# Optimization experiments

Hardware: AMD Instinct MI355X
Metric: run time of the kernel (lower is better)

Reference implementation:

```python
import jax, jax.numpy as jnp
import numpy as np
import math

NC = 80
TOPK = 10
EPS = 1e-9
DIS = 2.5
BIG = 1e5


def _ciou(b1, b2, eps=EPS):
    # b1: (bs,1,A,4), b2: (bs,G,1,4) -> (bs,G,A)
    b1x1, b1y1, b1x2, b1y2 = b1[..., 0], b1[..., 1], b1[..., 2], b1[..., 3]
    b2x1, b2y1, b2x2, b2y2 = b2[..., 0], b2[..., 1], b2[..., 2], b2[..., 3]
    w1, h1 = b1x2 - b1x1, b1y2 - b1y1 + eps
    w2, h2 = b2x2 - b2x1, b2y2 - b2y1 + eps
    iw = jnp.clip(jnp.minimum(b1x2, b2x2) - jnp.maximum(b1x1, b2x1), 0.0)
    ih = jnp.clip(jnp.minimum(b1y2, b2y2) - jnp.maximum(b1y1, b2y1), 0.0)
    inter = iw * ih
    union = w1 * h1 + w2 * h2 - inter + eps
    iou = inter / union
    cw = jnp.maximum(b1x2, b2x2) - jnp.minimum(b1x1, b2x1)
    ch = jnp.maximum(b1y2, b2y2) - jnp.minimum(b1y1, b2y1)
    c2 = cw * cw + ch * ch + eps
    d2 = ((b2x1 + b2x2 - b1x1 - b1x2) ** 2 + (b2y1 + b2y2 - b1y1 - b1y2) ** 2) / 4.0
    v = (4.0 / math.pi ** 2) * (jnp.arctan(w2 / h2) - jnp.arctan(w1 / h1)) ** 2
    alpha = jax.lax.stop_gradient(v / (v - iou + (1.0 + eps)))
    return iou - (d2 / c2 + v * alpha)


def _cost_matrix(pred_boxes, gt_boxes, mask_gt, pred_scores, gt_labels):
    # geometric candidate masks
    pc = (pred_boxes[..., :2] + pred_boxes[..., 2:]) / 2.0  # (bs,A,2) anchor centers
    pce = pc[:, None, :, :]                                  # (bs,1,A,2)
    in_boxes = jnp.all(pce > gt_boxes[:, :, None, :2], -1) & jnp.all(gt_boxes[:, :, None, 2:] > pce, -1)
    gcen = (gt_boxes[..., :2] + gt_boxes[..., 2:]) / 2.0
    in_centers = jnp.all(pce > (gcen - DIS)[:, :, None, :], -1) & jnp.all((gcen + DIS)[:, :, None, :] > pce, -1)
    both = in_boxes & in_centers                             # (bs,G,A)

    ciou_val = _ciou(pred_boxes[:, None, :, :], gt_boxes[:, :, None, :])  # (bs,G,A)

    # summed BCE over classes against one-hot(gt_label), without (bs,G,A,nc) intermediate:
    # sum_c bce = -sum_c log(1-p_c) - (log p_y - log(1-p_y))
    p = jnp.clip(pred_scores, 1e-7, 1.0 - 1e-7)
    logp = jnp.log(p)
    log1mp = jnp.log1p(-p)
    S = -log1mp.sum(-1)                                      # (bs,A)
    delta = -(logp - log1mp)                                 # (bs,A,nc)
    per_lab = jnp.take_along_axis(jnp.transpose(delta, (0, 2, 1)), gt_labels[:, :, None], axis=1)  # (bs,G,A)
    cls_cost = S[:, None, :] + per_lab

    cost = cls_cost + 3.0 * ciou_val + BIG * (~both).astype(cost_dtype(pred_boxes))
    return cost


def cost_dtype(x):
    return x.dtype


def reference(pred_boxes, gt_boxes, mask_gt, pred_scores, gt_labels):
    cost = _cost_matrix(pred_boxes, gt_boxes, mask_gt, pred_scores, gt_labels)  # (bs,G,A)
    bs, G, A = cost.shape
    # per-GT bottom-k (lowest cost) candidate anchors
    _, idx = jax.lax.top_k(-cost, TOPK)                      # (bs,G,TOPK)
    b_ix = jnp.arange(bs)[:, None, None]
    g_ix = jnp.arange(G)[None, :, None]
    pt_mask = jnp.zeros((bs, G, A), dtype=bool).at[b_ix, g_ix, idx].set(True)
    pt_mask = pt_mask & mask_gt[:, :, None]
    # conflict resolution: anchors claimed by >1 GT go to the min-cost GT
    overlap = pt_mask.sum(1) > 1                             # (bs,A)
    pick = jnp.argmin(jnp.where(pt_mask, cost, jnp.inf), axis=1)  # (bs,A)
    pick_oh = jnp.arange(G)[None, :, None] == pick[:, None, :]    # (bs,G,A)
    final = jnp.where(overlap[:, None, :], pick_oh, pt_mask) & mask_gt[:, :, None]
    return final, cost


def setup_inputs() -> dict:
    key = jax.random.key(0)
    k = jax.random.split(key, 7)
    bs, A, G = 32, 8400, 64
    pc = jax.random.uniform(k[0], (bs, A, 2)) * 640.0
    pwh = jax.random.uniform(k[1], (bs, A, 2)) * 96.0 + 8.0
    pred_boxes = jnp.concatenate([pc - pwh / 2, pc + pwh / 2], -1)
    gc = jax.random.uniform(k[2], (bs, G, 2)) * 640.0
    gwh = jax.random.uniform(k[3], (bs, G, 2)) * 128.0 + 16.0
    gt_boxes = jnp.concatenate([gc - gwh / 2, gc + gwh / 2], -1)
    mask_gt = jax.random.uniform(k[4], (bs, G)) < 0.8
    pred_scores = jax.random.uniform(k[5], (bs, A, NC), minval=1e-4, maxval=1.0 - 1e-4)
    gt_labels = jax.random.randint(k[6], (bs, G), 0, NC, dtype=jnp.int32)
    return {"pred_boxes": pred_boxes, "gt_boxes": gt_boxes, "mask_gt": mask_gt,
            "pred_scores": pred_scores, "gt_labels": gt_labels}
```

## Files before the change

kernel.cpp:

```cpp
#include <hip/hip_runtime.h>
#include <math.h>

#define BS   32
#define A_N  8400
#define G_N  64
#define NC_N 80
#define TK   10
#define DROWS 44

static __device__ __forceinline__ bool lexless(float v1, int i1, float v2, int i2) {
    return (v1 < v2) || (v1 == v2 && i1 < i2);
}
static __device__ __forceinline__ float fdiv(float n, float d) {
    return n * __builtin_amdgcn_rcpf(d);
}

__global__ __launch_bounds__(256)
void k_cost(const float* __restrict__ pred_boxes,
            const float* __restrict__ gt_boxes,
            const float* __restrict__ pred_scores,
            const int*   __restrict__ gt_labels,
            float* __restrict__ cost)
{
    __shared__ float s_gx1[G_N], s_gy1[G_N], s_gx2[G_N], s_gy2[G_N];
    __shared__ float s_gsx[G_N], s_gsy[G_N];
    __shared__ float s_glx[G_N], s_gly[G_N], s_ghx[G_N], s_ghy[G_N];
    __shared__ float s_area2[G_N], s_atg[G_N];
    __shared__ int   s_lab[G_N];
    __shared__ int   s_ord[G_N];
    __shared__ int   s_pres[NC_N];
    __shared__ int   s_rank[NC_N];
    __shared__ float s_delta[DROWS * 256];

    const float EPSF = 1e-9f;
    const int t = threadIdx.x;
    const int b = blockIdx.y;
    const int a = blockIdx.x * 256 + t;

    if (t < G_N) {
        const float4 gb = ((const float4*)gt_boxes)[b * G_N + t];
        const float gx1 = gb.x, gy1 = gb.y, gx2 = gb.z, gy2 = gb.w;
        s_gx1[t] = gx1; s_gy1[t] = gy1; s_gx2[t] = gx2; s_gy2[t] = gy2;
        const float sx = gx1 + gx2, sy = gy1 + gy2;
        s_gsx[t] = sx; s_gsy[t] = sy;
        const float cx = sx / 2.0f, cy = sy / 2.0f;
        s_glx[t] = cx - 2.5f; s_ghx[t] = cx + 2.5f;
        s_gly[t] = cy - 2.5f; s_ghy[t] = cy + 2.5f;
        const float w2 = gx2 - gx1;
        const float h2 = (gy2 - gy1) + EPSF;
        s_area2[t] = w2 * h2;
        s_atg[t]   = atanf(w2 / h2);
        s_lab[t]   = gt_labels[b * G_N + t];
    }
    __syncthreads();
    if (t < NC_N) {
        int pr = 0;
        for (int j = 0; j < G_N; ++j) pr |= (s_lab[j] == t);
        s_pres[t] = pr;
    }
    if (t < G_N) {
        const int myl = s_lab[t];
        int rank = 0;
        for (int j = 0; j < G_N; ++j) {
            const int lj = s_lab[j];
            rank += (lj < myl) || (lj == myl && j < t);
        }
        s_ord[rank] = t;
    }
    __syncthreads();
    if (t < NC_N) {
        int r = 0;
        for (int c = 0; c < t; ++c) r += s_pres[c];
        s_rank[t] = s_pres[t] ? r : -1;
    }
    __syncthreads();
    if (a >= A_N) return;

    const float* prow = pred_scores + ((size_t)b * A_N + a) * NC_N;
    const float LO = 1e-7f;
    const float HI = (float)(1.0 - 1e-7);
    float prod = 1.0f, Sacc = 0.0f;
    {
        const float4* p4 = (const float4*)prow;
        for (int c4 = 0; c4 < NC_N / 4; ++c4) {
            const float4 pv = p4[c4];
            const float ps[4] = {pv.x, pv.y, pv.z, pv.w};
            #pragma unroll
            for (int j = 0; j < 4; ++j) {
                const float pc = fminf(fmaxf(ps[j], LO), HI);
                const float q  = 1.0f - pc;
                prod *= q;
                const int r = s_rank[c4 * 4 + j];
                if (r >= 0 && r < DROWS)
                    s_delta[r * 256 + t] = logf(q * __builtin_amdgcn_rcpf(pc));
            }
            if (c4 & 1) { Sacc += logf(prod); prod = 1.0f; }
        }
    }
    const float S = -Sacc;

    const float4 pb = ((const float4*)pred_boxes)[(size_t)b * A_N + a];
    const float pcx  = (pb.x + pb.z) / 2.0f;
    const float pcy  = (pb.y + pb.w) / 2.0f;
    const float w1   = pb.z - pb.x;
    const float h1   = (pb.w - pb.y) + EPSF;
    const float area1 = w1 * h1;
    const float atp  = atanf(w1 / h1);
    const float KPI  = (float)(4.0 / (M_PI * M_PI));

    float* crow = cost + (size_t)b * G_N * A_N + a;
    int   cur_c = -1, krank = -1;
    float delta_c = 0.0f;
    for (int k = 0; k < G_N; ++k) {
        const int g = s_ord[k];
        const int c = s_lab[g];
        if (c != cur_c) {
            ++krank;
            if (krank < DROWS) {
                delta_c = s_delta[krank * 256 + t];
            } else {
                const float pc = fminf(fmaxf(prow[c], LO), HI);
                delta_c = logf((1.0f - pc) * __builtin_amdgcn_rcpf(pc));
            }
            cur_c = c;
        }

        const float gx1 = s_gx1[g], gy1 = s_gy1[g], gx2 = s_gx2[g], gy2 = s_gy2[g];
        const bool inb  = (pcx > gx1) && (pcy > gy1) && (gx2 > pcx) && (gy2 > pcy);
        const bool inc  = (pcx > s_glx[g]) && (pcy > s_gly[g]) &&
                          (s_ghx[g] > pcx) && (s_ghy[g] > pcy);
        const bool both = inb && inc;

        const float iw    = fmaxf(fminf(pb.z, gx2) - fmaxf(pb.x, gx1), 0.0f);
        const float ih    = fmaxf(fminf(pb.w, gy2) - fmaxf(pb.y, gy1), 0.0f);
        const float inter = iw * ih;
        const float uni   = ((area1 + s_area2[g]) - inter) + EPSF;
        const float iou   = fdiv(inter, uni);
        const float cw    = fmaxf(pb.z, gx2) - fminf(pb.x, gx1);
        const float ch    = fmaxf(pb.w, gy2) - fminf(pb.y, gy1);
        const float c2    = ((cw * cw) + (ch * ch)) + EPSF;
        const float dx    = (s_gsx[g] - pb.x) - pb.z;
        const float dy    = (s_gsy[g] - pb.y) - pb.w;
        const float d2    = ((dx * dx) + (dy * dy)) / 4.0f;
        const float dif   = s_atg[g] - atp;
        const float v     = KPI * (dif * dif);
        const float alpha = fdiv(v, (v - iou) + 1.0f);
        const float ciou  = iou - (fdiv(d2, c2) + v * alpha);

        const float cls   = S + delta_c;
        const float cst   = (cls + 3.0f * ciou) + (both ? 0.0f : 100000.0f);
        crow[(size_t)g * A_N] = cst;
    }
}

__global__ __launch_bounds__(256)
void k_topk(const float* __restrict__ cost, int* __restrict__ topk)
{
    __shared__ float s_wv[4][TK];
    __shared__ int   s_wi[4][TK];

    const int bg   = blockIdx.x;
    const int t    = threadIdx.x;
    const int lane = t & 63;
    const int wid  = t >> 6;
    const float* row = cost + (size_t)bg * A_N;
    const float FINF = __builtin_inff();

    float v[TK]; int id[TK];
    #pragma unroll
    for (int j = 0; j < TK; ++j) { v[j] = FINF; id[j] = 0x7FFFFFFF; }

    auto consider = [&](float c, int a) {
        if (lexless(c, a, v[TK - 1], id[TK - 1])) {
            v[TK - 1] = c; id[TK - 1] = a;
            #pragma unroll
            for (int j = TK - 2; j >= 0; --j) {
                const bool sw = lexless(v[j + 1], id[j + 1], v[j], id[j]);
                const float tv = v[j]; const int ti = id[j];
                v[j]      = sw ? v[j + 1] : v[j];
                id[j]     = sw ? id[j + 1] : id[j];
                v[j + 1]  = sw ? tv : v[j + 1];
                id[j + 1] = sw ? ti : id[j + 1];
            }
        }
    };

    const float4* row4 = (const float4*)row;
    for (int i = t; i < A_N / 4; i += 256) {
        const float4 c4 = row4[i];
        const int base = i * 4;
        consider(c4.x, base);
        consider(c4.y, base + 1);
        consider(c4.z, base + 2);
        consider(c4.w, base + 3);
    }

    #pragma unroll
    for (int r = 0; r < TK; ++r) {
        float bv = v[0]; int ba = id[0];
        #pragma unroll
        for (int off = 1; off < 64; off <<= 1) {
            const float ov = __shfl_xor(bv, off, 64);
            const int   oa = __shfl_xor(ba, off, 64);
            if (lexless(ov, oa, bv, ba)) { bv = ov; ba = oa; }
        }
        if (lane == 0) { s_wv[wid][r] = bv; s_wi[wid][r] = ba; }
        if (id[0] == ba) {
            #pragma unroll
            for (int j = 0; j < TK - 1; ++j) { v[j] = v[j + 1]; id[j] = id[j + 1]; }
            v[TK - 1] = FINF; id[TK - 1] = 0x7FFFFFFF;
        }
    }
    __syncthreads();

    if (wid == 0) {
        float cv = FINF; int ci = 0x7FFFFFFF;
        if (lane < 4 * TK) { cv = s_wv[lane / TK][lane % TK]; ci = s_wi[lane / TK][lane % TK]; }
        #pragma unroll
        for (int r = 0; r < TK; ++r) {
            float bv = cv; int ba = ci;
            #pragma unroll
            for (int off = 1; off < 64; off <<= 1) {
                const float ov = __shfl_xor(bv, off, 64);
                const int   oa = __shfl_xor(ba, off, 64);
                if (lexless(ov, oa, bv, ba)) { bv = ov; ba = oa; }
            }
            if (lane == 0) topk[bg * TK + r] = ba;
            if (ci == ba) { cv = FINF; ci = 0x7FFFFFFF; }
        }
    }
}

__global__ __launch_bounds__(256)
void k_final(const float* __restrict__ cost,
             const int*   __restrict__ topk,
             const unsigned char* __restrict__ mask_gt,
             float* __restrict__ final_out)
{
    __shared__ int s_top[G_N * TK];
    __shared__ int s_mask[G_N];

    const int t = threadIdx.x;
    const int b = blockIdx.y;
    const int a = blockIdx.x * 256 + t;

    for (int k = t; k < G_N * TK; k += 256) s_top[k] = topk[b * G_N * TK + k];
    if (t < G_N) s_mask[t] = (int)mask_gt[b * G_N + t];
    __syncthreads();
    if (a >= A_N) return;

    unsigned long long member = 0ull;
    int cnt = 0;
    float best = __builtin_inff();
    int bestg = 0;
    for (int g = 0; g < G_N; ++g) {
        bool m = false;
        if (s_mask[g]) {
            #pragma unroll
            for (int j = 0; j < TK; ++j) m = m || (s_top[g * TK + j] == a);
        }
        if (m) {
            member |= (1ull << g);
            ++cnt;
            const float c = cost[((size_t)b * G_N + g) * A_N + a];
            if (c < best) { best = c; bestg = g; }
        }
    }
    const bool ovl = cnt > 1;
    float* frow = final_out + (size_t)b * G_N * A_N + a;
    for (int g = 0; g < G_N; ++g) {
        const bool f = ovl ? (g == bestg) : (((member >> g) & 1ull) != 0ull);
        frow[(size_t)g * A_N] = f ? 1.0f : 0.0f;
    }
}

extern "C" void kernel_launch(void* const* d_in, const int* in_sizes, int n_in,
                              void* d_out, int out_size, void* d_ws, size_t ws_size,
                              hipStream_t stream)
{
    const float* pred_boxes  = (const float*)d_in[0];
    const float* gt_boxes    = (const float*)d_in[1];
    const unsigned char* mask_gt = (const unsigned char*)d_in[2];
    const float* pred_scores = (const float*)d_in[3];
    const int*   gt_labels   = (const int*)d_in[4];

    float* out_final = (float*)d_out;
    float* out_cost  = out_final + (size_t)BS * G_N * A_N;
    int*   topk_ws   = (int*)d_ws;

    k_cost <<<dim3((A_N + 255) / 256, BS), 256, 0, stream>>>(
        pred_boxes, gt_boxes, pred_scores, gt_labels, out_cost);
    k_topk <<<dim3(BS * G_N), 256, 0, stream>>>(out_cost, topk_ws);
    k_final<<<dim3((A_N + 255) / 256, BS), 256, 0, stream>>>(
        out_cost, topk_ws, mask_gt, out_final);
}
```

Baseline: 355.2 us.

## Replace dense final-mask pass with sparse atomic scatter and shrink delta LDS

The dense k_final pass, which read the whole cost matrix, is replaced by a memset of the output plus two small scatter kernels over only the top-k candidates. An atomicMin on a packed key of sortable cost and gt index resolves anchors claimed by several gts. Separately, the LDS delta buffer is halved and refilled in chunks by re-reading the scores row, and k_cost gets a min-blocks-per-SM launch bound to raise occupancy. Risks are extra launches, atomic contention, and relying on the workspace being large enough, with a fallback to the old kernel if it is not.

After: 365.8 us. 1.03x slower.

```diff
diff --git a/kernel.cpp b/kernel.cpp
--- a/kernel.cpp
+++ b/kernel.cpp
@@ -6,7 +6,7 @@
 #define G_N  64
 #define NC_N 80
 #define TK   10
-#define DROWS 44
+#define DROWS 22
 
 static __device__ __forceinline__ bool lexless(float v1, int i1, float v2, int i2) {
     return (v1 < v2) || (v1 == v2 && i1 < i2);
@@ -14,8 +14,12 @@
 static __device__ __forceinline__ float fdiv(float n, float d) {
     return n * __builtin_amdgcn_rcpf(d);
 }
-
-__global__ __launch_bounds__(256)
+static __device__ __forceinline__ unsigned sortable(float f) {
+    unsigned u = __float_as_uint(f);
+    return (u & 0x80000000u) ? ~u : (u | 0x80000000u);
+}
+
+__global__ __launch_bounds__(256, 6)
 void k_cost(const float* __restrict__ pred_boxes,
             const float* __restrict__ gt_boxes,
             const float* __restrict__ pred_scores,
@@ -77,25 +81,24 @@
     if (a >= A_N) return;
 
     const float* prow = pred_scores + ((size_t)b * A_N + a) * NC_N;
+    const float4* p4 = (const float4*)prow;
     const float LO = 1e-7f;
     const float HI = (float)(1.0 - 1e-7);
+
     float prod = 1.0f, Sacc = 0.0f;
-    {
-        const float4* p4 = (const float4*)prow;
-        for (int c4 = 0; c4 < NC_N / 4; ++c4) {
-            const float4 pv = p4[c4];
-            const float ps[4] = {pv.x, pv.y, pv.z, pv.w};
-            #pragma unroll
-            for (int j = 0; j < 4; ++j) {
-                const float pc = fminf(fmaxf(ps[j], LO), HI);
-                const float q  = 1.0f - pc;
-                prod *= q;
-                const int r = s_rank[c4 * 4 + j];
-                if (r >= 0 && r < DROWS)
-                    s_delta[r * 256 + t] = logf(q * __builtin_amdgcn_rcpf(pc));
-            }
-            if (c4 & 1) { Sacc += logf(prod); prod = 1.0f; }
-        }
+    for (int c4 = 0; c4 < NC_N / 4; ++c4) {
+        const float4 pv = p4[c4];
+        const float ps[4] = {pv.x, pv.y, pv.z, pv.w};
+        #pragma unroll
+        for (int j = 0; j < 4; ++j) {
+            const float pc = fminf(fmaxf(ps[j], LO), HI);
+            const float q  = 1.0f - pc;
+            prod *= q;
+            const int r = s_rank[c4 * 4 + j];
+            if (r >= 0 && r < DROWS)
+                s_delta[r * 256 + t] = logf(q * __builtin_amdgcn_rcpf(pc));
+        }
+        if (c4 & 1) { Sacc += logf(prod); prod = 1.0f; }
     }
     const float S = -Sacc;
 
@@ -109,19 +112,30 @@
     const float KPI  = (float)(4.0 / (M_PI * M_PI));
 
     float* crow = cost + (size_t)b * G_N * A_N + a;
-    int   cur_c = -1, krank = -1;
+    int   cur_c = -1, krank = -1, base = 0;
     float delta_c = 0.0f;
     for (int k = 0; k < G_N; ++k) {
         const int g = s_ord[k];
         const int c = s_lab[g];
         if (c != cur_c) {
             ++krank;
-            if (krank < DROWS) {
-                delta_c = s_delta[krank * 256 + t];
-            } else {
-                const float pc = fminf(fmaxf(prow[c], LO), HI);
-                delta_c = logf((1.0f - pc) * __builtin_amdgcn_rcpf(pc));
+            if (krank >= base + DROWS) {
+                base += DROWS;
+                for (int c4 = 0; c4 < NC_N / 4; ++c4) {
+                    const float4 pv = p4[c4];
+                    const float ps[4] = {pv.x, pv.y, pv.z, pv.w};
+                    #pragma unroll
+                    for (int j = 0; j < 4; ++j) {
+                        const int r = s_rank[c4 * 4 + j];
+                        if (r >= base && r < base + DROWS) {
+                            const float pc = fminf(fmaxf(ps[j], LO), HI);
+                            s_delta[(r - base) * 256 + t] =
+                                logf((1.0f - pc) * __builtin_amdgcn_rcpf(pc));
+                        }
+                    }
+                }
             }
+            delta_c = s_delta[(krank - base) * 256 + t];
             cur_c = c;
         }
 
@@ -232,6 +246,41 @@
 }
 
 __global__ __launch_bounds__(256)
+void k_scatter1(const float* __restrict__ cost,
+                const int*   __restrict__ topk,
+                const unsigned char* __restrict__ mask_gt,
+                unsigned long long* __restrict__ slot)
+{
+    const int e = blockIdx.x * 256 + threadIdx.x;
+    if (e >= BS * G_N * TK) return;
+    const int b = e / (G_N * TK);
+    const int r = e % (G_N * TK);
+    const int g = r / TK;
+    if (!mask_gt[b * G_N + g]) return;
+    const int a = topk[e];
+    const float c = cost[((size_t)b * G_N + g) * A_N + a];
+    const unsigned long long key = ((unsigned long long)sortable(c) << 6) | (unsigned)g;
+    atomicMin(&slot[(size_t)b * A_N + a], key);
+}
+
+__global__ __launch_bounds__(256)
+void k_scatter2(const int* __restrict__ topk,
+                const unsigned char* __restrict__ mask_gt,
+                const unsigned long long* __restrict__ slot,
+                float* __restrict__ final_out)
+{
+    const int e = blockIdx.x * 256 + threadIdx.x;
+    if (e >= BS * G_N * TK) return;
+    const int b = e / (G_N * TK);
+    const int r = e % (G_N * TK);
+    const int g = r / TK;
+    if (!mask_gt[b * G_N + g]) return;
+    const int a = topk[e];
+    if ((int)(slot[(size_t)b * A_N + a] & 63ull) == g)
+        final_out[((size_t)b * G_N + g) * A_N + a] = 1.0f;
+}
+
+__global__ __launch_bounds__(256)
 void k_final(const float* __restrict__ cost,
              const int*   __restrict__ topk,
              const unsigned char* __restrict__ mask_gt,
@@ -286,11 +335,28 @@
 
     float* out_final = (float*)d_out;
     float* out_cost  = out_final + (size_t)BS * G_N * A_N;
-    int*   topk_ws   = (int*)d_ws;
+
+    const size_t slot_bytes = (size_t)BS * A_N * sizeof(unsigned long long);
+    const size_t topk_bytes = (size_t)BS * G_N * TK * sizeof(int);
+    unsigned long long* slot = (unsigned long long*)d_ws;
+    int* topk_ws = (int*)((char*)d_ws + slot_bytes);
+    const bool sparse_ok = ws_size >= slot_bytes + topk_bytes;
+    if (!sparse_ok) topk_ws = (int*)d_ws;
 
     k_cost <<<dim3((A_N + 255) / 256, BS), 256, 0, stream>>>(
         pred_boxes, gt_boxes, pred_scores, gt_labels, out_cost);
     k_topk <<<dim3(BS * G_N), 256, 0, stream>>>(out_cost, topk_ws);
-    k_final<<<dim3((A_N + 255) / 256, BS), 256, 0, stream>>>(
-        out_cost, topk_ws, mask_gt, out_final);
-}
+
+    if (sparse_ok) {
+        hipMemsetAsync(out_final, 0, (size_t)BS * G_N * A_N * sizeof(float), stream);
+        hipMemsetAsync(slot, 0xFF, slot_bytes, stream);
+        const int NE = BS * G_N * TK;
+        k_scatter1<<<dim3((NE + 255) / 256), 256, 0, stream>>>(
+            out_cost, topk_ws, mask_gt, slot);
+        k_scatter2<<<dim3((NE + 255) / 256), 256, 0, stream>>>(
+            topk_ws, mask_gt, slot, out_final);
+    } else {
+        k_final<<<dim3((A_N + 255) / 256, BS), 256, 0, stream>>>(
+            out_cost, topk_ws, mask_gt, out_final);
+    }
+}
```
